# Kernel tuning notes

Hardware: AMD Instinct MI355X
Metric: run time of the kernel (lower is better)

## Reference

```python
import jax, jax.numpy as jnp
import numpy as np

S, N, P = 128, 512, 92
DIM_IN = P + N  # 604
DIMS = [128, 128, 128]
HID = 256
HEADS = [100, 1, 1, 1]


def _lin(key, fan_in, fan_out):
    kw, kb = jax.random.split(key)
    s = 1.0 / np.sqrt(fan_in)
    W = jax.random.uniform(kw, (fan_in, fan_out), jnp.float32, -s, s)
    b = jax.random.uniform(kb, (fan_out,), jnp.float32, -s, s)
    return W, b


def setup_inputs() -> dict:
    key = jax.random.key(0)
    ks = jax.random.split(key, 16)
    node_feat = jax.random.normal(ks[0], (S, N, P), jnp.float32)
    bond_feat = jax.random.normal(ks[1], (S, N, N), jnp.float32)
    # sparse symmetric adjacency, ~degree 25 per node
    a = jax.random.uniform(ks[2], (S, N, N)) < 0.025
    connectivity = (a | jnp.transpose(a, (0, 2, 1))).astype(jnp.int32)
    batchAssign = jnp.repeat(jnp.arange(S, dtype=jnp.int32), N)  # (S*N,)
    W0, b0 = _lin(ks[3], DIM_IN, DIMS[0])
    W1, b1 = _lin(ks[4], DIMS[0], DIMS[1])
    W2, b2 = _lin(ks[5], DIMS[1], DIMS[2])
    Wh, bh = _lin(ks[6], DIMS[2], HID)
    Wi, bi = _lin(ks[7], HID, HEADS[0])
    We, be = _lin(ks[8], HID, HEADS[1])
    Wlb, blb = _lin(ks[9], HID, HEADS[2])
    Wub, bub = _lin(ks[10], HID, HEADS[3])
    return dict(node_feat=node_feat, bond_feat=bond_feat, connectivity=connectivity,
                batchAssign=batchAssign, W0=W0, b0=b0, W1=W1, b1=b1, W2=W2, b2=b2,
                Wh=Wh, bh=bh, Wi=Wi, bi=bi, We=We, be=be, Wlb=Wlb, blb=blb,
                Wub=Wub, bub=bub)


def _gcn_norm(connectivity, dtype):
    # PyG GCNConv: add self loops, norm = d^{-1/2}[src] * d^{-1/2}[dst],
    # deg counted at target (column) index; src=row, trg=col of connectivity.
    n = connectivity.shape[-1]
    Ahat = (connectivity != 0).astype(dtype) + jnp.eye(n, dtype=dtype)
    deg = Ahat.sum(axis=1)              # (S,N) in-degree at column j (>=1)
    dinv = jax.lax.rsqrt(deg)
    return Ahat * dinv[:, :, None] * dinv[:, None, :]  # (S,N,N)


def reference(node_feat, bond_feat, connectivity, batchAssign,
              W0, b0, W1, b1, W2, b2, Wh, bh, Wi, bi, We, be, Wlb, blb, Wub, bub):
    n = node_feat.shape[1]
    x = jnp.concatenate([node_feat, bond_feat[:, :n, :n]], axis=-1)  # (S,N,P+N)
    An = _gcn_norm(connectivity, x.dtype)
    for W, b in ((W0, b0), (W1, b1), (W2, b2)):
        # out[t] = sum_s Anorm[s->t] * (x W)[s]  (propagate src->trg)
        x = jnp.einsum('sij,sif->sjf', An, x @ W) + b
    s = connectivity.shape[0]
    pooled = jax.ops.segment_sum(x.reshape(s * n, -1), batchAssign, num_segments=s)
    h = jax.nn.softplus(pooled) @ Wh + bh
    return (h @ Wi + bi, h @ We + be, h @ Wlb + blb, h @ Wub + bub)
```

## Files before the change

kernel.cpp:

```cpp
#include <hip/hip_runtime.h>
#include <hip/hip_bf16.h>
#include <math.h>

#define S 128
#define N 512
#define P 92
#define DIN 604
#define KPAD0 608
#define D 128
#define HID 256
#define MAXDEG 64

typedef __attribute__((ext_vector_type(8))) short frag8;
typedef __attribute__((ext_vector_type(4))) float floatx4;

__device__ inline void split1(float x, unsigned short& h, unsigned short& l) {
    __hip_bfloat16 hb = __float2bfloat16(x);
    float hf = __bfloat162float(hb);
    __hip_bfloat16 lb = __float2bfloat16(x - hf);
    h = *(unsigned short*)&hb;
    l = *(unsigned short*)&lb;
}

__global__ void k_pre(const int* __restrict__ conn,
                      unsigned short* __restrict__ idx,
                      int* __restrict__ degs,
                      float* __restrict__ dinv,
                      float* __restrict__ pooled) {
    int zidx = blockIdx.x * 256 + (int)threadIdx.x;
    if (zidx < S * D) pooled[zidx] = 0.f;

    int row  = blockIdx.x * 4 + (threadIdx.x >> 6);
    int lane = threadIdx.x & 63;
    const int* r = conn + (size_t)row * N;
    unsigned short* irow = idx + (size_t)row * MAXDEG;
    int deg = 0;
#pragma unroll
    for (int w = 0; w < 8; ++w) {
        int c = r[w * 64 + lane];
        unsigned long long bits = __ballot(c != 0);
        int below = __popcll(bits & ((1ull << lane) - 1ull));
        if (c != 0) {
            int pos = deg + below;
            if (pos < MAXDEG) irow[pos] = (unsigned short)(w * 64 + lane);
        }
        deg += __popcll(bits);
    }
    if (lane == 0) {
        degs[row] = deg < MAXDEG ? deg : MAXDEG;
        dinv[row] = rsqrtf((float)(deg + 1));
    }
}

__global__ void k_wt(const float* __restrict__ W, int K, int Kpad,
                     unsigned short* __restrict__ th, unsigned short* __restrict__ tl) {
    int i = blockIdx.x * 256 + threadIdx.x;
    if (i >= Kpad * 128) return;
    int k = i >> 7, n = i & 127;
    float v = (k < K) ? W[(size_t)k * 128 + n] : 0.f;
    unsigned short h, l;
    split1(v, h, l);
    th[(size_t)n * Kpad + k] = h;
    tl[(size_t)n * Kpad + k] = l;
}

__global__ __launch_bounds__(128) void k_y0_mfma(
    const float* __restrict__ nf, const float* __restrict__ bfm,
    const unsigned short* __restrict__ w0th, const unsigned short* __restrict__ w0tl,
    const float* __restrict__ dinv, float* __restrict__ y)
{
    __shared__ __align__(16) unsigned short As_hi[64][32], As_lo[64][32];
    __shared__ __align__(16) unsigned short Bs_hi[128][32], Bs_lo[128][32];
    int s  = blockIdx.y;
    int m0 = blockIdx.x * 64;
    int tid = threadIdx.x;
    int lane = tid & 63, w = tid >> 6;
    int lr = lane & 15, q = lane >> 4;
    const float* nfs = nf  + (size_t)s * N * P;
    const float* bfs = bfm + (size_t)s * N * N;

    floatx4 acc[2][8];
#pragma unroll
    for (int r = 0; r < 2; ++r)
#pragma unroll
        for (int c = 0; c < 8; ++c)
            acc[r][c] = (floatx4){0.f, 0.f, 0.f, 0.f};

    for (int kc = 0; kc < KPAD0 / 32; ++kc) {
        int k0 = kc * 32;
#pragma unroll
        for (int l = 0; l < 4; ++l) {
            int i2 = tid + l * 128;
            int row = i2 >> 3, q4 = i2 & 7;
            int k = k0 + q4 * 4;
            int m = m0 + row;
            float4 v = make_float4(0.f, 0.f, 0.f, 0.f);
            if (k < P)        v = *(const float4*)(nfs + (size_t)m * P + k);
            else if (k < DIN) v = *(const float4*)(bfs + (size_t)m * N + (k - P));
            ushort4 h, lo;
            split1(v.x, h.x, lo.x); split1(v.y, h.y, lo.y);
            split1(v.z, h.z, lo.z); split1(v.w, h.w, lo.w);
            *(ushort4*)&As_hi[row][q4 * 4] = h;
            *(ushort4*)&As_lo[row][q4 * 4] = lo;
        }
#pragma unroll
        for (int l = 0; l < 4; ++l) {
            int i2 = tid + l * 128;
            int n = i2 >> 2, q8 = i2 & 3;
            *(uint4*)&Bs_hi[n][q8 * 8] = *(const uint4*)(w0th + (size_t)n * KPAD0 + k0 + q8 * 8);
            *(uint4*)&Bs_lo[n][q8 * 8] = *(const uint4*)(w0tl + (size_t)n * KPAD0 + k0 + q8 * 8);
        }
        __syncthreads();
        frag8 a_h[2], a_l[2];
        a_h[0] = *(const frag8*)&As_hi[32 * w + lr][q * 8];
        a_h[1] = *(const frag8*)&As_hi[32 * w + 16 + lr][q * 8];
        a_l[0] = *(const frag8*)&As_lo[32 * w + lr][q * 8];
        a_l[1] = *(const frag8*)&As_lo[32 * w + 16 + lr][q * 8];
#pragma unroll
        for (int c = 0; c < 8; ++c) {
            frag8 b_h = *(const frag8*)&Bs_hi[16 * c + lr][q * 8];
            frag8 b_l = *(const frag8*)&Bs_lo[16 * c + lr][q * 8];
#pragma unroll
            for (int r = 0; r < 2; ++r) {
                acc[r][c] = __builtin_amdgcn_mfma_f32_16x16x32_bf16(a_h[r], b_h, acc[r][c], 0, 0, 0);
                acc[r][c] = __builtin_amdgcn_mfma_f32_16x16x32_bf16(a_l[r], b_h, acc[r][c], 0, 0, 0);
                acc[r][c] = __builtin_amdgcn_mfma_f32_16x16x32_bf16(a_h[r], b_l, acc[r][c], 0, 0, 0);
            }
        }
        __syncthreads();
    }
#pragma unroll
    for (int r = 0; r < 2; ++r) {
        int mb = m0 + 32 * w + 16 * r + 4 * q;
#pragma unroll
        for (int reg = 0; reg < 4; ++reg) {
            int m = mb + reg;
            float dv = dinv[s * N + m];
            float* yr = y + ((size_t)s * N + m) * D;
#pragma unroll
            for (int c = 0; c < 8; ++c)
                yr[16 * c + lr] = acc[r][c][reg] * dv;
        }
    }
}

__global__ __launch_bounds__(128) void k_xw_mfma(
    const float* __restrict__ zin,
    const unsigned short* __restrict__ wth, const unsigned short* __restrict__ wtl,
    const float* __restrict__ dinv, float* __restrict__ y)
{
    __shared__ __align__(16) unsigned short As_hi[64][32], As_lo[64][32];
    __shared__ __align__(16) unsigned short Bs_hi[128][32], Bs_lo[128][32];
    int m0 = blockIdx.x * 64;
    int tid = threadIdx.x;
    int lane = tid & 63, w = tid >> 6;
    int lr = lane & 15, q = lane >> 4;

    floatx4 acc[2][8];
#pragma unroll
    for (int r = 0; r < 2; ++r)
#pragma unroll
        for (int c = 0; c < 8; ++c)
            acc[r][c] = (floatx4){0.f, 0.f, 0.f, 0.f};

    for (int kc = 0; kc < D / 32; ++kc) {
        int k0 = kc * 32;
#pragma unroll
        for (int l = 0; l < 4; ++l) {
            int i2 = tid + l * 128;
            int row = i2 >> 3, q4 = i2 & 7;
            float4 v = *(const float4*)(zin + (size_t)(m0 + row) * D + k0 + q4 * 4);
            ushort4 h, lo;
            split1(v.x, h.x, lo.x); split1(v.y, h.y, lo.y);
            split1(v.z, h.z, lo.z); split1(v.w, h.w, lo.w);
            *(ushort4*)&As_hi[row][q4 * 4] = h;
            *(ushort4*)&As_lo[row][q4 * 4] = lo;
        }
#pragma unroll
        for (int l = 0; l < 4; ++l) {
            int i2 = tid + l * 128;
            int n = i2 >> 2, q8 = i2 & 3;
            *(uint4*)&Bs_hi[n][q8 * 8] = *(const uint4*)(wth + (size_t)n * D + k0 + q8 * 8);
            *(uint4*)&Bs_lo[n][q8 * 8] = *(const uint4*)(wtl + (size_t)n * D + k0 + q8 * 8);
        }
        __syncthreads();
        frag8 a_h[2], a_l[2];
        a_h[0] = *(const frag8*)&As_hi[32 * w + lr][q * 8];
        a_h[1] = *(const frag8*)&As_hi[32 * w + 16 + lr][q * 8];
        a_l[0] = *(const frag8*)&As_lo[32 * w + lr][q * 8];
        a_l[1] = *(const frag8*)&As_lo[32 * w + 16 + lr][q * 8];
#pragma unroll
        for (int c = 0; c < 8; ++c) {
            frag8 b_h = *(const frag8*)&Bs_hi[16 * c + lr][q * 8];
            frag8 b_l = *(const frag8*)&Bs_lo[16 * c + lr][q * 8];
#pragma unroll
            for (int r = 0; r < 2; ++r) {
                acc[r][c] = __builtin_amdgcn_mfma_f32_16x16x32_bf16(a_h[r], b_h, acc[r][c], 0, 0, 0);
                acc[r][c] = __builtin_amdgcn_mfma_f32_16x16x32_bf16(a_l[r], b_h, acc[r][c], 0, 0, 0);
                acc[r][c] = __builtin_amdgcn_mfma_f32_16x16x32_bf16(a_h[r], b_l, acc[r][c], 0, 0, 0);
            }
        }
        __syncthreads();
    }
#pragma unroll
    for (int r = 0; r < 2; ++r) {
        int mb = m0 + 32 * w + 16 * r + 4 * q;
#pragma unroll
        for (int reg = 0; reg < 4; ++reg) {
            int m = mb + reg;
            float dv = dinv[m];
            float* yr = y + (size_t)m * D;
#pragma unroll
            for (int c = 0; c < 8; ++c)
                yr[16 * c + lr] = acc[r][c][reg] * dv;
        }
    }
}

__global__ __launch_bounds__(256) void k_prop_csr(
    const unsigned short* __restrict__ idx, const int* __restrict__ degs,
    const float* __restrict__ dinv,
    const float* __restrict__ yin, const float* __restrict__ bias,
    float* __restrict__ z, float* __restrict__ pooled)
{
    __shared__ unsigned short sidx[8][MAXDEG];
    __shared__ int sdeg[8];
    int s  = blockIdx.y;
    int g  = threadIdx.x >> 5;
    int j  = blockIdx.x * 8 + g;
    int f4 = threadIdx.x & 31;
    const float* ys = yin + (size_t)s * N * D;

    {
        int tg = threadIdx.x >> 5, pair = threadIdx.x & 31;
        const unsigned int* src = (const unsigned int*)(idx + ((size_t)(s * N + blockIdx.x * 8 + tg)) * MAXDEG);
        ((unsigned int*)&sidx[tg][0])[pair] = src[pair];
        if (threadIdx.x < 8) sdeg[threadIdx.x] = degs[s * N + blockIdx.x * 8 + threadIdx.x];
    }
    __syncthreads();

    float4 acc = *(const float4*)(ys + (size_t)j * D + f4 * 4);
    int d = sdeg[g];
    int b = 0;
    for (; b + 8 <= d; b += 8) {
        float4 v[8];
#pragma unroll
        for (int qq = 0; qq < 8; ++qq) {
            int i = sidx[g][b + qq];
            v[qq] = *(const float4*)(ys + (size_t)i * D + f4 * 4);
        }
#pragma unroll
        for (int qq = 0; qq < 8; ++qq) {
            acc.x += v[qq].x; acc.y += v[qq].y; acc.z += v[qq].z; acc.w += v[qq].w;
        }
    }
    for (; b < d; ++b) {
        int i = sidx[g][b];
        float4 v = *(const float4*)(ys + (size_t)i * D + f4 * 4);
        acc.x += v.x; acc.y += v.y; acc.z += v.z; acc.w += v.w;
    }

    float dv = dinv[s * N + j];
    int f = f4 * 4;
    float4 r = { acc.x * dv + bias[f],     acc.y * dv + bias[f + 1],
                 acc.z * dv + bias[f + 2], acc.w * dv + bias[f + 3] };

    if (pooled == nullptr) {
        *(float4*)(z + ((size_t)s * N + j) * D + f) = r;
    } else {
        __shared__ float red[8][D];
        *(float4*)&red[g][f] = r;
        __syncthreads();
        if (threadIdx.x < D) {
            float t = 0.f;
#pragma unroll
            for (int qq = 0; qq < 8; ++qq) t += red[qq][threadIdx.x];
            atomicAdd(pooled + s * D + threadIdx.x, t);
        }
    }
}

__global__ __launch_bounds__(256) void k_head(
    const float* __restrict__ pooled,
    const float* __restrict__ Wh, const float* __restrict__ bh,
    const float* __restrict__ Wi, const float* __restrict__ bi,
    const float* __restrict__ We, const float* __restrict__ be,
    const float* __restrict__ Wlb, const float* __restrict__ blb,
    const float* __restrict__ Wub, const float* __restrict__ bub,
    float* __restrict__ out)
{
    int s = blockIdx.x;
    int t = threadIdx.x;
    __shared__ float sp[D];
    __shared__ float h[HID];
    if (t < D) {
        float x = pooled[s * D + t];
        sp[t] = (x > 20.f) ? x : log1pf(expf(x));
    }
    __syncthreads();
    {
        float a = bh[t];
        for (int g = 0; g < D; ++g)
            a += sp[g] * Wh[g * HID + t];
        h[t] = a;
    }
    __syncthreads();
    if (t < 100) {
        float a = bi[t];
        for (int k = 0; k < HID; ++k)
            a += h[k] * Wi[k * 100 + t];
        out[s * 100 + t] = a;
    } else if (t < 103) {
        const float* Wv = (t == 100) ? We : (t == 101) ? Wlb : Wub;
        float bv = (t == 100) ? be[0] : (t == 101) ? blb[0] : bub[0];
        float a = bv;
        for (int k = 0; k < HID; ++k)
            a += h[k] * Wv[k];
        out[S * 100 + (t - 100) * S + s] = a;
    }
}

extern "C" void kernel_launch(void* const* d_in, const int* in_sizes, int n_in,
                              void* d_out, int out_size, void* d_ws, size_t ws_size,
                              hipStream_t stream) {
    const float* nf   = (const float*)d_in[0];
    const float* bfm  = (const float*)d_in[1];
    const int*   conn = (const int*)d_in[2];
    const float* W0 = (const float*)d_in[4];
    const float* b0 = (const float*)d_in[5];
    const float* W1 = (const float*)d_in[6];
    const float* b1 = (const float*)d_in[7];
    const float* W2 = (const float*)d_in[8];
    const float* b2 = (const float*)d_in[9];
    const float* Wh = (const float*)d_in[10];
    const float* bh = (const float*)d_in[11];
    const float* Wi = (const float*)d_in[12];
    const float* bi = (const float*)d_in[13];
    const float* We = (const float*)d_in[14];
    const float* be = (const float*)d_in[15];
    const float* Wlb = (const float*)d_in[16];
    const float* blb = (const float*)d_in[17];
    const float* Wub = (const float*)d_in[18];
    const float* bub = (const float*)d_in[19];
    float* out = (float*)d_out;

    char* ws = (char*)d_ws;
    float* ybuf = (float*)ws;
    float* zbuf = (float*)(ws + (1u << 25));
    char* base2 = ws + (1u << 26);
    float* dinv = (float*)(base2);
    int*   degs = (int*)(base2 + 0x40000);
    float* pooled = (float*)(base2 + 0x80000);
    unsigned short* idx = (unsigned short*)(base2 + 0x90000);
    unsigned short* w0th = (unsigned short*)(base2 + 0x890000);
    unsigned short* w0tl = (unsigned short*)(base2 + 0x8D0000);
    unsigned short* w1th = (unsigned short*)(base2 + 0x910000);
    unsigned short* w1tl = (unsigned short*)(base2 + 0x920000);
    unsigned short* w2th = (unsigned short*)(base2 + 0x930000);
    unsigned short* w2tl = (unsigned short*)(base2 + 0x940000);

    k_pre<<<S * N / 4, 256, 0, stream>>>(conn, idx, degs, dinv, pooled);
    k_wt<<<(KPAD0 * 128 + 255) / 256, 256, 0, stream>>>(W0, DIN, KPAD0, w0th, w0tl);
    k_wt<<<(D * 128 + 255) / 256, 256, 0, stream>>>(W1, D, D, w1th, w1tl);
    k_wt<<<(D * 128 + 255) / 256, 256, 0, stream>>>(W2, D, D, w2th, w2tl);

    k_y0_mfma<<<dim3(N / 64, S), 128, 0, stream>>>(nf, bfm, w0th, w0tl, dinv, ybuf);
    k_prop_csr<<<dim3(N / 8, S), 256, 0, stream>>>(idx, degs, dinv, ybuf, b0, zbuf, nullptr);
    k_xw_mfma<<<S * N / 64, 128, 0, stream>>>(zbuf, w1th, w1tl, dinv, ybuf);
    k_prop_csr<<<dim3(N / 8, S), 256, 0, stream>>>(idx, degs, dinv, ybuf, b1, zbuf, nullptr);
    k_xw_mfma<<<S * N / 64, 128, 0, stream>>>(zbuf, w2th, w2tl, dinv, ybuf);
    k_prop_csr<<<dim3(N / 8, S), 256, 0, stream>>>(idx, degs, dinv, ybuf, b2, zbuf, pooled);
    k_head<<<S, 256, 0, stream>>>(pooled, Wh, bh, Wi, bi, We, be, Wlb, blb, Wub, bub, out);
}
```

Baseline: 615.9 us.

## Prefetch GEMM tiles into registers, pre-swizzle weights, pad CSR neighbor lists

The MFMA GEMM kernels now prefetch A and B tiles into registers one or two K-chunks ahead, so global loads overlap with MFMA work. Weights are pre-split into a fragment-ordered layout so B tiles are copied contiguously and read with lane-linear LDS access, and the A tile rows are padded to 40 to reduce bank conflicts. The CSR builder reads connectivity with int4 loads and pads each neighbor list to a multiple of 8 with self-indices. The propagate kernel then drops its scalar tail loop and subtracts the padded self contributions afterwards. The cost is more registers held for prefetch, which may lower occupancy, plus a few extra gathers per row.

Result: slower. 781.7 us (+26.9%).

```diff
diff --git a/kernel.cpp b/kernel.cpp
--- a/kernel.cpp
+++ b/kernel.cpp
@@ -6,11 +6,13 @@
 #define N 512
 #define P 92
 #define DIN 604
-#define KPAD0 608
+#define KC0 19
 #define D 128
+#define KC1 4
 #define HID 256
 #define MAXDEG 64
 
+typedef unsigned short ushort_t;
 typedef __attribute__((ext_vector_type(8))) short frag8;
 typedef __attribute__((ext_vector_type(4))) float floatx4;
 
@@ -32,49 +34,70 @@
 
     int row  = blockIdx.x * 4 + (threadIdx.x >> 6);
     int lane = threadIdx.x & 63;
-    const int* r = conn + (size_t)row * N;
+    const int4* r = (const int4*)(conn + (size_t)row * N);
     unsigned short* irow = idx + (size_t)row * MAXDEG;
     int deg = 0;
 #pragma unroll
-    for (int w = 0; w < 8; ++w) {
-        int c = r[w * 64 + lane];
-        unsigned long long bits = __ballot(c != 0);
-        int below = __popcll(bits & ((1ull << lane) - 1ull));
-        if (c != 0) {
-            int pos = deg + below;
-            if (pos < MAXDEG) irow[pos] = (unsigned short)(w * 64 + lane);
-        }
-        deg += __popcll(bits);
+    for (int it = 0; it < 2; ++it) {
+        int4 c = r[it * 64 + lane];
+        int col0 = it * 256 + lane * 4;
+#pragma unroll
+        for (int comp = 0; comp < 4; ++comp) {
+            int cv = (comp == 0) ? c.x : (comp == 1) ? c.y : (comp == 2) ? c.z : c.w;
+            unsigned long long bits = __ballot(cv != 0);
+            int below = __popcll(bits & ((1ull << lane) - 1ull));
+            if (cv != 0) {
+                int pos = deg + below;
+                if (pos < MAXDEG) irow[pos] = (unsigned short)(col0 + comp);
+            }
+            deg += __popcll(bits);
+        }
     }
     if (lane == 0) {
-        degs[row] = deg < MAXDEG ? deg : MAXDEG;
-        dinv[row] = rsqrtf((float)(deg + 1));
-    }
-}
-
-__global__ void k_wt(const float* __restrict__ W, int K, int Kpad,
+        float dv = rsqrtf((float)(deg + 1));
+        if (deg > MAXDEG) deg = MAXDEG;
+        int padded = (deg + 7) & ~7;
+        for (int p = deg; p < padded; ++p) irow[p] = (unsigned short)(row & (N - 1));
+        degs[row] = padded | ((padded - deg) << 16);
+        dinv[row] = dv;
+    }
+}
+
+__global__ void k_wt(const float* __restrict__ W, int K, int KC,
                      unsigned short* __restrict__ th, unsigned short* __restrict__ tl) {
-    int i = blockIdx.x * 256 + threadIdx.x;
-    if (i >= Kpad * 128) return;
-    int k = i >> 7, n = i & 127;
-    float v = (k < K) ? W[(size_t)k * 128 + n] : 0.f;
-    unsigned short h, l;
-    split1(v, h, l);
-    th[(size_t)n * Kpad + k] = h;
-    tl[(size_t)n * Kpad + k] = l;
+    int t = blockIdx.x * 256 + (int)threadIdx.x;
+    if (t >= KC * 512) return;
+    int lane = t & 63, c = (t >> 6) & 7, kc = t >> 9;
+    int lr = lane & 15, q = lane >> 4;
+    int n = 16 * c + lr;
+    ushort4 h0, h1, l0, l1;
+    unsigned short hh[8], ll[8];
+#pragma unroll
+    for (int j = 0; j < 8; ++j) {
+        int k = kc * 32 + q * 8 + j;
+        float v = (k < K) ? W[(size_t)k * 128 + n] : 0.f;
+        split1(v, hh[j], ll[j]);
+    }
+    h0 = make_ushort4(hh[0], hh[1], hh[2], hh[3]);
+    h1 = make_ushort4(hh[4], hh[5], hh[6], hh[7]);
+    l0 = make_ushort4(ll[0], ll[1], ll[2], ll[3]);
+    l1 = make_ushort4(ll[4], ll[5], ll[6], ll[7]);
+    *(ushort4*)(th + (size_t)t * 8)     = h0;
+    *(ushort4*)(th + (size_t)t * 8 + 4) = h1;
+    *(ushort4*)(tl + (size_t)t * 8)     = l0;
+    *(ushort4*)(tl + (size_t)t * 8 + 4) = l1;
 }
 
 __global__ __launch_bounds__(128) void k_y0_mfma(
     const float* __restrict__ nf, const float* __restrict__ bfm,
-    const unsigned short* __restrict__ w0th, const unsigned short* __restrict__ w0tl,
+    const unsigned short* __restrict__ w0fh, const unsigned short* __restrict__ w0fl,
     const float* __restrict__ dinv, float* __restrict__ y)
 {
-    __shared__ __align__(16) unsigned short As_hi[64][32], As_lo[64][32];
-    __shared__ __align__(16) unsigned short Bs_hi[128][32], Bs_lo[128][32];
+    __shared__ __align__(16) unsigned short AsH[64][40], AsL[64][40];
+    __shared__ __align__(16) unsigned short BsH[4096], BsL[4096];
     int s  = blockIdx.y;
     int m0 = blockIdx.x * 64;
-    int tid = threadIdx.x;
-    int lane = tid & 63, w = tid >> 6;
+    int tid = threadIdx.x, lane = tid & 63, w = tid >> 6;
     int lr = lane & 15, q = lane >> 4;
     const float* nfs = nf  + (size_t)s * N * P;
     const float* bfs = bfm + (size_t)s * N * N;
@@ -86,40 +109,66 @@
         for (int c = 0; c < 8; ++c)
             acc[r][c] = (floatx4){0.f, 0.f, 0.f, 0.f};
 
-    for (int kc = 0; kc < KPAD0 / 32; ++kc) {
-        int k0 = kc * 32;
+    float4 pa[2][4];
+    uint4 pbh[4], pbl[4];
+
+#define LOAD_A(kc, dst)                                                      \
+    {                                                                        \
+        int k0_ = (kc) * 32;                                                 \
+        _Pragma("unroll")                                                    \
+        for (int l = 0; l < 4; ++l) {                                        \
+            int i2 = tid + l * 128;                                          \
+            int row = i2 >> 3, q4 = i2 & 7;                                  \
+            int k = k0_ + q4 * 4, m = m0 + row;                              \
+            float4 v = make_float4(0.f, 0.f, 0.f, 0.f);                      \
+            if (k < P)        v = *(const float4*)(nfs + (size_t)m * P + k); \
+            else if (k < DIN) v = *(const float4*)(bfs + (size_t)m * N + (k - P)); \
+            (dst)[l] = v;                                                    \
+        }                                                                    \
+    }
+#define LOAD_B(kc)                                                           \
+    {                                                                        \
+        const unsigned short* bh_ = w0fh + (size_t)(kc) * 4096;              \
+        const unsigned short* bl_ = w0fl + (size_t)(kc) * 4096;              \
+        _Pragma("unroll")                                                    \
+        for (int l = 0; l < 4; ++l) {                                        \
+            pbh[l] = *(const uint4*)(bh_ + (size_t)(tid + l * 128) * 8);     \
+            pbl[l] = *(const uint4*)(bl_ + (size_t)(tid + l * 128) * 8);     \
+        }                                                                    \
+    }
+
+    LOAD_A(0, pa[0]);
+    LOAD_B(0);
+    LOAD_A(1, pa[1]);
+
+    for (int kc = 0; kc < KC0; ++kc) {
+        int cur = kc & 1;
 #pragma unroll
         for (int l = 0; l < 4; ++l) {
             int i2 = tid + l * 128;
             int row = i2 >> 3, q4 = i2 & 7;
-            int k = k0 + q4 * 4;
-            int m = m0 + row;
-            float4 v = make_float4(0.f, 0.f, 0.f, 0.f);
-            if (k < P)        v = *(const float4*)(nfs + (size_t)m * P + k);
-            else if (k < DIN) v = *(const float4*)(bfs + (size_t)m * N + (k - P));
+            float4 v = pa[cur][l];
             ushort4 h, lo;
             split1(v.x, h.x, lo.x); split1(v.y, h.y, lo.y);
             split1(v.z, h.z, lo.z); split1(v.w, h.w, lo.w);
-            *(ushort4*)&As_hi[row][q4 * 4] = h;
-            *(ushort4*)&As_lo[row][q4 * 4] = lo;
-        }
-#pragma unroll
-        for (int l = 0; l < 4; ++l) {
-            int i2 = tid + l * 128;
-            int n = i2 >> 2, q8 = i2 & 3;
-            *(uint4*)&Bs_hi[n][q8 * 8] = *(const uint4*)(w0th + (size_t)n * KPAD0 + k0 + q8 * 8);
-            *(uint4*)&Bs_lo[n][q8 * 8] = *(const uint4*)(w0tl + (size_t)n * KPAD0 + k0 + q8 * 8);
+            *(ushort4*)&AsH[row][q4 * 4] = h;
+            *(ushort4*)&AsL[row][q4 * 4] = lo;
+            *(uint4*)&BsH[(size_t)i2 * 8] = pbh[l];
+            *(uint4*)&BsL[(size_t)i2 * 8] = pbl[l];
         }
         __syncthreads();
+        if (kc + 1 < KC0) LOAD_B(kc + 1);
+        if (kc + 2 < KC0) LOAD_A(kc + 2, pa[cur]);
+
         frag8 a_h[2], a_l[2];
-        a_h[0] = *(const frag8*)&As_hi[32 * w + lr][q * 8];
-        a_h[1] = *(const frag8*)&As_hi[32 * w + 16 + lr][q * 8];
-        a_l[0] = *(const frag8*)&As_lo[32 * w + lr][q * 8];
-        a_l[1] = *(const frag8*)&As_lo[32 * w + 16 + lr][q * 8];
+        a_h[0] = *(const frag8*)&AsH[32 * w + lr][q * 8];
+        a_h[1] = *(const frag8*)&AsH[32 * w + 16 + lr][q * 8];
+        a_l[0] = *(const frag8*)&AsL[32 * w + lr][q * 8];
+        a_l[1] = *(const frag8*)&AsL[32 * w + 16 + lr][q * 8];
 #pragma unroll
         for (int c = 0; c < 8; ++c) {
-            frag8 b_h = *(const frag8*)&Bs_hi[16 * c + lr][q * 8];
-            frag8 b_l = *(const frag8*)&Bs_lo[16 * c + lr][q * 8];
+            frag8 b_h = *(const frag8*)&BsH[(c * 64 + lane) * 8];
+            frag8 b_l = *(const frag8*)&BsL[(c * 64 + lane) * 8];
 #pragma unroll
             for (int r = 0; r < 2; ++r) {
                 acc[r][c] = __builtin_amdgcn_mfma_f32_16x16x32_bf16(a_h[r], b_h, acc[r][c], 0, 0, 0);
@@ -129,6 +178,8 @@
         }
         __syncthreads();
     }
+#undef LOAD_A
+#undef LOAD_B
 #pragma unroll
     for (int r = 0; r < 2; ++r) {
         int mb = m0 + 32 * w + 16 * r + 4 * q;
@@ -146,14 +197,13 @@
 
 __global__ __launch_bounds__(128) void k_xw_mfma(
     const float* __restrict__ zin,
-    const unsigned short* __restrict__ wth, const unsigned short* __restrict__ wtl,
+    const unsigned short* __restrict__ wfh, const unsigned short* __restrict__ wfl,
     const float* __restrict__ dinv, float* __restrict__ y)
 {
-    __shared__ __align__(16) unsigned short As_hi[64][32], As_lo[64][32];
-    __shared__ __align__(16) unsigned short Bs_hi[128][32], Bs_lo[128][32];
+    __shared__ __align__(16) unsigned short AsH[64][40], AsL[64][40];
+    __shared__ __align__(16) unsigned short BsH[4096], BsL[4096];
     int m0 = blockIdx.x * 64;
-    int tid = threadIdx.x;
-    int lane = tid & 63, w = tid >> 6;
+    int tid = threadIdx.x, lane = tid & 63, w = tid >> 6;
     int lr = lane & 15, q = lane >> 4;
 
     floatx4 acc[2][8];
@@ -163,36 +213,62 @@
         for (int c = 0; c < 8; ++c)
             acc[r][c] = (floatx4){0.f, 0.f, 0.f, 0.f};
 
-    for (int kc = 0; kc < D / 32; ++kc) {
-        int k0 = kc * 32;
+    float4 pa[2][4];
+    uint4 pbh[4], pbl[4];
+
+#define LOAD_A(kc, dst)                                                      \
+    {                                                                        \
+        int k0_ = (kc) * 32;                                                 \
+        _Pragma("unroll")                                                    \
+        for (int l = 0; l < 4; ++l) {                                        \
+            int i2 = tid + l * 128;                                          \
+            int row = i2 >> 3, q4 = i2 & 7;                                  \
+            (dst)[l] = *(const float4*)(zin + (size_t)(m0 + row) * D + k0_ + q4 * 4); \
+        }                                                                    \
+    }
+#define LOAD_B(kc)                                                           \
+    {                                                                        \
+        const unsigned short* bh_ = wfh + (size_t)(kc) * 4096;               \
+        const unsigned short* bl_ = wfl + (size_t)(kc) * 4096;               \
+        _Pragma("unroll")                                                    \
+        for (int l = 0; l < 4; ++l) {                                        \
+            pbh[l] = *(const uint4*)(bh_ + (size_t)(tid + l * 128) * 8);     \
+            pbl[l] = *(const uint4*)(bl_ + (size_t)(tid + l * 128) * 8);     \
+        }                                                                    \
+    }
+
+    LOAD_A(0, pa[0]);
+    LOAD_B(0);
+    LOAD_A(1, pa[1]);
+
+    for (int kc = 0; kc < KC1; ++kc) {
+        int cur = kc & 1;
 #pragma unroll
         for (int l = 0; l < 4; ++l) {
             int i2 = tid + l * 128;
             int row = i2 >> 3, q4 = i2 & 7;
-            float4 v = *(const float4*)(zin + (size_t)(m0 + row) * D + k0 + q4 * 4);
+            float4 v = pa[cur][l];
             ushort4 h, lo;
             split1(v.x, h.x, lo.x); split1(v.y, h.y, lo.y);
             split1(v.z, h.z, lo.z); split1(v.w, h.w, lo.w);
-            *(ushort4*)&As_hi[row][q4 * 4] = h;
-            *(ushort4*)&As_lo[row][q4 * 4] = lo;
-        }
-#pragma unroll
-        for (int l = 0; l < 4; ++l) {
-            int i2 = tid + l * 128;
-            int n = i2 >> 2, q8 = i2 & 3;
-            *(uint4*)&Bs_hi[n][q8 * 8] = *(const uint4*)(wth + (size_t)n * D + k0 + q8 * 8);
-            *(uint4*)&Bs_lo[n][q8 * 8] = *(const uint4*)(wtl + (size_t)n * D + k0 + q8 * 8);
+            *(ushort4*)&AsH[row][q4 * 4] = h;
+            *(ushort4*)&AsL[row][q4 * 4] = lo;
+            *(uint4*)&BsH[(size_t)i2 * 8] = pbh[l];
+            *(uint4*)&BsL[(size_t)i2 * 8] = pbl[l];
         }
         __syncthreads();
+        if (kc + 1 < KC1) LOAD_B(kc + 1);
+        if (kc + 2 < KC1) LOAD_A(kc + 2, pa[cur]);
+
         frag8 a_h[2], a_l[2];
-        a_h[0] = *(const frag8*)&As_hi[32 * w + lr][q * 8];
-        a_h[1] = *(const frag8*)&As_hi[32 * w + 16 + lr][q * 8];
-        a_l[0] = *(const frag8*)&As_lo[32 * w + lr][q * 8];
-        a_l[1] = *(const frag8*)&As_lo[32 * w + 16 + lr][q * 8];
+        a_h[0] = *(const frag8*)&AsH[32 * w + lr][q * 8];
+        a_h[1] = *(const frag8*)&AsH[32 * w + 16 + lr][q * 8];
+        a_l[0] = *(const frag8*)&AsL[32 * w + lr][q * 8];
+        a_l[1] = *(const frag8*)&AsL[32 * w + 16 + lr][q * 8];
 #pragma unroll
         for (int c = 0; c < 8; ++c) {
-            frag8 b_h = *(const frag8*)&Bs_hi[16 * c + lr][q * 8];
-            frag8 b_l = *(const frag8*)&Bs_lo[16 * c + lr][q * 8];
+            frag8 b_h = *(const frag8*)&BsH[(c * 64 + lane) * 8];
+            frag8 b_l = *(const frag8*)&BsL[(c * 64 + lane) * 8];
 #pragma unroll
             for (int r = 0; r < 2; ++r) {
                 acc[r][c] = __builtin_amdgcn_mfma_f32_16x16x32_bf16(a_h[r], b_h, acc[r][c], 0, 0, 0);
@@ -202,6 +278,8 @@
         }
         __syncthreads();
     }
+#undef LOAD_A
+#undef LOAD_B
 #pragma unroll
     for (int r = 0; r < 2; ++r) {
         int mb = m0 + 32 * w + 16 * r + 4 * q;
@@ -239,10 +317,11 @@
     }
     __syncthreads();
 
-    float4 acc = *(const float4*)(ys + (size_t)j * D + f4 * 4);
-    int d = sdeg[g];
-    int b = 0;
-    for (; b + 8 <= d; b += 8) {
+    float4 yj = *(const float4*)(ys + (size_t)j * D + f4 * 4);
+    float4 acc = yj;
+    int dp = sdeg[g];
+    int d = dp & 0xffff, pads = dp >> 16;
+    for (int b = 0; b < d; b += 8) {
         float4 v[8];
 #pragma unroll
         for (int qq = 0; qq < 8; ++qq) {
@@ -254,11 +333,8 @@
             acc.x += v[qq].x; acc.y += v[qq].y; acc.z += v[qq].z; acc.w += v[qq].w;
         }
     }
-    for (; b < d; ++b) {
-        int i = sidx[g][b];
-        float4 v = *(const float4*)(ys + (size_t)i * D + f4 * 4);
-        acc.x += v.x; acc.y += v.y; acc.z += v.z; acc.w += v.w;
-    }
+    float fp = (float)pads;
+    acc.x -= fp * yj.x; acc.y -= fp * yj.y; acc.z -= fp * yj.z; acc.w -= fp * yj.w;
 
     float dv = dinv[s * N + j];
     int f = f4 * 4;
@@ -352,23 +428,23 @@
     int*   degs = (int*)(base2 + 0x40000);
     float* pooled = (float*)(base2 + 0x80000);
     unsigned short* idx = (unsigned short*)(base2 + 0x90000);
-    unsigned short* w0th = (unsigned short*)(base2 + 0x890000);
-    unsigned short* w0tl = (unsigned short*)(base2 + 0x8D0000);
-    unsigned short* w1th = (unsigned short*)(base2 + 0x910000);
-    unsigned short* w1tl = (unsigned short*)(base2 + 0x920000);
-    unsigned short* w2th = (unsigned short*)(base2 + 0x930000);
-    unsigned short* w2tl = (unsigned short*)(base2 + 0x940000);
+    unsigned short* w0fh = (unsigned short*)(base2 + 0x890000);
+    unsigned short* w0fl = (unsigned short*)(base2 + 0x8C0000);
+    unsigned short* w1fh = (unsigned short*)(base2 + 0x8F0000);
+    unsigned short* w1fl = (unsigned short*)(base2 + 0x900000);
+    unsigned short* w2fh = (unsigned short*)(base2 + 0x910000);
+    unsigned short* w2fl = (unsigned short*)(base2 + 0x920000);
 
     k_pre<<<S * N / 4, 256, 0, stream>>>(conn, idx, degs, dinv, pooled);
-    k_wt<<<(KPAD0 * 128 + 255) / 256, 256, 0, stream>>>(W0, DIN, KPAD0, w0th, w0tl);
-    k_wt<<<(D * 128 + 255) / 256, 256, 0, stream>>>(W1, D, D, w1th, w1tl);
-    k_wt<<<(D * 128 + 255) / 256, 256, 0, stream>>>(W2, D, D, w2th, w2tl);
-
-    k_y0_mfma<<<dim3(N / 64, S), 128, 0, stream>>>(nf, bfm, w0th, w0tl, dinv, ybuf);
+    k_wt<<<(KC0 * 512 + 255) / 256, 256, 0, stream>>>(W0, DIN, KC0, w0fh, w0fl);
+    k_wt<<<(KC1 * 512 + 255) / 256, 256, 0, stream>>>(W1, D, KC1, w1fh, w1fl);
+    k_wt<<<(KC1 * 512 + 255) / 256, 256, 0, stream>>>(W2, D, KC1, w2fh, w2fl);
+
+    k_y0_mfma<<<dim3(N / 64, S), 128, 0, stream>>>(nf, bfm, w0fh, w0fl, dinv, ybuf);
     k_prop_csr<<<dim3(N / 8, S), 256, 0, stream>>>(idx, degs, dinv, ybuf, b0, zbuf, nullptr);
-    k_xw_mfma<<<S * N / 64, 128, 0, stream>>>(zbuf, w1th, w1tl, dinv, ybuf);
+    k_xw_mfma<<<S * N / 64, 128, 0, stream>>>(zbuf, w1fh, w1fl, dinv, ybuf);
     k_prop_csr<<<dim3(N / 8, S), 256, 0, stream>>>(idx, degs, dinv, ybuf, b1, zbuf, nullptr);
-    k_xw_mfma<<<S * N / 64, 128, 0, stream>>>(zbuf, w2th, w2tl, dinv, ybuf);
+    k_xw_mfma<<<S * N / 64, 128, 0, stream>>>(zbuf, w2fh, w2fl, dinv, ybuf);
     k_prop_csr<<<dim3(N / 8, S), 256, 0, stream>>>(idx, degs, dinv, ybuf, b2, zbuf, pooled);
     k_head<<<S, 256, 0, stream>>>(pooled, Wh, bh, Wi, bi, We, be, Wlb, blb, Wub, bub, out);
 }
```

## Remap propagation blocks per XCD, pad neighbor lists, vectorize adjacency scan

Applied to the files above, without the earlier changes.

The adjacency scan in k_pre now reads int4 vectors. Each neighbor list is padded to a multiple of 8 with self-indices, and the pad count is stored so it can be subtracted later. The propagation kernel now handles 64 nodes per block with 8 per thread group. Block indices are remapped so all blocks for one graph land on the same XCD, which should improve L2 reuse of that graph's features. Pooling is accumulated in registers before one atomic per feature per block, which removes the remainder loop and cuts the number of atomics, at the cost of fewer and larger blocks.

After: 589.6 us. -4.3%, faster.

```diff
diff --git a/kernel.cpp b/kernel.cpp
--- a/kernel.cpp
+++ b/kernel.cpp
@@ -32,23 +32,32 @@
 
     int row  = blockIdx.x * 4 + (threadIdx.x >> 6);
     int lane = threadIdx.x & 63;
-    const int* r = conn + (size_t)row * N;
+    const int4* r = (const int4*)(conn + (size_t)row * N);
     unsigned short* irow = idx + (size_t)row * MAXDEG;
     int deg = 0;
 #pragma unroll
-    for (int w = 0; w < 8; ++w) {
-        int c = r[w * 64 + lane];
-        unsigned long long bits = __ballot(c != 0);
-        int below = __popcll(bits & ((1ull << lane) - 1ull));
-        if (c != 0) {
-            int pos = deg + below;
-            if (pos < MAXDEG) irow[pos] = (unsigned short)(w * 64 + lane);
-        }
-        deg += __popcll(bits);
+    for (int it = 0; it < 2; ++it) {
+        int4 c = r[it * 64 + lane];
+        int col0 = it * 256 + lane * 4;
+#pragma unroll
+        for (int comp = 0; comp < 4; ++comp) {
+            int cv = (comp == 0) ? c.x : (comp == 1) ? c.y : (comp == 2) ? c.z : c.w;
+            unsigned long long bits = __ballot(cv != 0);
+            int below = __popcll(bits & ((1ull << lane) - 1ull));
+            if (cv != 0) {
+                int pos = deg + below;
+                if (pos < MAXDEG) irow[pos] = (unsigned short)(col0 + comp);
+            }
+            deg += __popcll(bits);
+        }
     }
     if (lane == 0) {
-        degs[row] = deg < MAXDEG ? deg : MAXDEG;
-        dinv[row] = rsqrtf((float)(deg + 1));
+        float dv = rsqrtf((float)(deg + 1));
+        if (deg > MAXDEG) deg = MAXDEG;
+        int padded = (deg + 7) & ~7;
+        for (int p = deg; p < padded; ++p) irow[p] = (unsigned short)(row & (N - 1));
+        degs[row] = padded | ((padded - deg) << 16);
+        dinv[row] = dv;
     }
 }
 
@@ -217,65 +226,76 @@
     }
 }
 
-__global__ __launch_bounds__(256) void k_prop_csr(
+__global__ __launch_bounds__(256) void k_prop_xcd(
     const unsigned short* __restrict__ idx, const int* __restrict__ degs,
     const float* __restrict__ dinv,
     const float* __restrict__ yin, const float* __restrict__ bias,
     float* __restrict__ z, float* __restrict__ pooled)
 {
-    __shared__ unsigned short sidx[8][MAXDEG];
-    __shared__ int sdeg[8];
-    int s  = blockIdx.y;
-    int g  = threadIdx.x >> 5;
-    int j  = blockIdx.x * 8 + g;
-    int f4 = threadIdx.x & 31;
+    __shared__ unsigned short sidx[64][MAXDEG];
+    __shared__ int sdeg[64];
+    __shared__ float red[8][D];
+    int b = blockIdx.x;
+    int s   = ((b & 7) << 4) | ((b >> 3) & 15);
+    int sub = (b >> 7) & 7;
+    int j0 = sub * 64;
+    int tid = threadIdx.x;
     const float* ys = yin + (size_t)s * N * D;
 
     {
-        int tg = threadIdx.x >> 5, pair = threadIdx.x & 31;
-        const unsigned int* src = (const unsigned int*)(idx + ((size_t)(s * N + blockIdx.x * 8 + tg)) * MAXDEG);
-        ((unsigned int*)&sidx[tg][0])[pair] = src[pair];
-        if (threadIdx.x < 8) sdeg[threadIdx.x] = degs[s * N + blockIdx.x * 8 + threadIdx.x];
+        const unsigned int* src = (const unsigned int*)(idx + ((size_t)s * N + j0) * MAXDEG);
+        unsigned int* dst = (unsigned int*)&sidx[0][0];
+#pragma unroll
+        for (int l = 0; l < 8; ++l) dst[tid + l * 256] = src[tid + l * 256];
+        if (tid < 64) sdeg[tid] = degs[s * N + j0 + tid];
     }
     __syncthreads();
 
-    float4 acc = *(const float4*)(ys + (size_t)j * D + f4 * 4);
-    int d = sdeg[g];
-    int b = 0;
-    for (; b + 8 <= d; b += 8) {
-        float4 v[8];
-#pragma unroll
-        for (int qq = 0; qq < 8; ++qq) {
-            int i = sidx[g][b + qq];
-            v[qq] = *(const float4*)(ys + (size_t)i * D + f4 * 4);
-        }
-#pragma unroll
-        for (int qq = 0; qq < 8; ++qq) {
-            acc.x += v[qq].x; acc.y += v[qq].y; acc.z += v[qq].z; acc.w += v[qq].w;
-        }
-    }
-    for (; b < d; ++b) {
-        int i = sidx[g][b];
-        float4 v = *(const float4*)(ys + (size_t)i * D + f4 * 4);
-        acc.x += v.x; acc.y += v.y; acc.z += v.z; acc.w += v.w;
-    }
-
-    float dv = dinv[s * N + j];
-    int f = f4 * 4;
-    float4 r = { acc.x * dv + bias[f],     acc.y * dv + bias[f + 1],
-                 acc.z * dv + bias[f + 2], acc.w * dv + bias[f + 3] };
-
-    if (pooled == nullptr) {
-        *(float4*)(z + ((size_t)s * N + j) * D + f) = r;
-    } else {
-        __shared__ float red[8][D];
-        *(float4*)&red[g][f] = r;
-        __syncthreads();
-        if (threadIdx.x < D) {
+    int g = tid >> 5, f4 = tid & 31, f = f4 * 4;
+    float4 bias4 = *(const float4*)(bias + f);
+    float4 pacc = make_float4(0.f, 0.f, 0.f, 0.f);
+
+#pragma unroll
+    for (int jj = 0; jj < 8; ++jj) {
+        int jl = jj * 8 + g;
+        int j = j0 + jl;
+        float4 yj = *(const float4*)(ys + (size_t)j * D + f);
+        float4 acc = yj;
+        int dp = sdeg[jl];
+        int d = dp & 0xffff, pads = dp >> 16;
+        for (int bb = 0; bb < d; bb += 8) {
+            float4 v[8];
+#pragma unroll
+            for (int qq = 0; qq < 8; ++qq) {
+                int i = sidx[jl][bb + qq];
+                v[qq] = *(const float4*)(ys + (size_t)i * D + f);
+            }
+#pragma unroll
+            for (int qq = 0; qq < 8; ++qq) {
+                acc.x += v[qq].x; acc.y += v[qq].y; acc.z += v[qq].z; acc.w += v[qq].w;
+            }
+        }
+        float fp = (float)pads;
+        acc.x -= fp * yj.x; acc.y -= fp * yj.y; acc.z -= fp * yj.z; acc.w -= fp * yj.w;
+
+        float dv = dinv[s * N + j];
+        float4 r = { acc.x * dv + bias4.x, acc.y * dv + bias4.y,
+                     acc.z * dv + bias4.z, acc.w * dv + bias4.w };
+        if (pooled == nullptr) {
+            *(float4*)(z + ((size_t)s * N + j) * D + f) = r;
+        } else {
+            pacc.x += r.x; pacc.y += r.y; pacc.z += r.z; pacc.w += r.w;
+        }
+    }
+
+    if (pooled != nullptr) {
+        *(float4*)&red[g][f] = pacc;
+        __syncthreads();
+        if (tid < D) {
             float t = 0.f;
 #pragma unroll
-            for (int qq = 0; qq < 8; ++qq) t += red[qq][threadIdx.x];
-            atomicAdd(pooled + s * D + threadIdx.x, t);
+            for (int qq = 0; qq < 8; ++qq) t += red[qq][tid];
+            atomicAdd(pooled + s * D + tid, t);
         }
     }
 }
@@ -365,10 +385,10 @@
     k_wt<<<(D * 128 + 255) / 256, 256, 0, stream>>>(W2, D, D, w2th, w2tl);
 
     k_y0_mfma<<<dim3(N / 64, S), 128, 0, stream>>>(nf, bfm, w0th, w0tl, dinv, ybuf);
-    k_prop_csr<<<dim3(N / 8, S), 256, 0, stream>>>(idx, degs, dinv, ybuf, b0, zbuf, nullptr);
+    k_prop_xcd<<<S * 8, 256, 0, stream>>>(idx, degs, dinv, ybuf, b0, zbuf, nullptr);
     k_xw_mfma<<<S * N / 64, 128, 0, stream>>>(zbuf, w1th, w1tl, dinv, ybuf);
-    k_prop_csr<<<dim3(N / 8, S), 256, 0, stream>>>(idx, degs, dinv, ybuf, b1, zbuf, nullptr);
+    k_prop_xcd<<<S * 8, 256, 0, stream>>>(idx, degs, dinv, ybuf, b1, zbuf, nullptr);
     k_xw_mfma<<<S * N / 64, 128, 0, stream>>>(zbuf, w2th, w2tl, dinv, ybuf);
-    k_prop_csr<<<dim3(N / 8, S), 256, 0, stream>>>(idx, degs, dinv, ybuf, b2, zbuf, pooled);
+    k_prop_xcd<<<S * 8, 256, 0, stream>>>(idx, degs, dinv, ybuf, b2, zbuf, pooled);
     k_head<<<S, 256, 0, stream>>>(pooled, Wh, bh, Wi, bi, We, be, Wlb, blb, Wub, bub, out);
 }
```
